# Performance work log

Hardware: AMD Instinct MI355X
Metric: run time of the kernel (lower is better)

## Reference

```python
import jax, jax.numpy as jnp
import numpy as np

BLOCK_SIZE = 256


def setup_inputs() -> dict:
    key = jax.random.key(0)
    k1, k2, k3, k4 = jax.random.split(key, 4)
    B, T, C, H = 512, 256, 384, 64
    x = jax.random.normal(k1, (B, T, C), dtype=jnp.float32)
    Wk = jax.random.normal(k2, (H, C), dtype=jnp.float32) * (1.0 / np.sqrt(C))
    Wq = jax.random.normal(k3, (H, C), dtype=jnp.float32) * (1.0 / np.sqrt(C))
    Wv = jax.random.normal(k4, (H, C), dtype=jnp.float32) * (1.0 / np.sqrt(C))
    return {"x": x, "Wk": Wk, "Wq": Wq, "Wv": Wv}


def reference(x, Wk, Wq, Wv):
    # x: [B, T, C]; Wk/Wq/Wv: [H, C] (torch nn.Linear weight layout, bias=False)
    B, T, C = x.shape
    H = Wk.shape[0]
    k = jnp.einsum('btc,hc->bth', x, Wk)
    q = jnp.einsum('btc,hc->bth', x, Wq)
    v = jnp.einsum('btc,hc->bth', x, Wv)
    scale = 1.0 / jnp.sqrt(jnp.float32(H))
    scores = jnp.einsum('bqh,bkh->bqk', q, k) * scale  # [B, T, T]
    causal = jnp.tril(jnp.ones((T, T), dtype=bool))
    scores = jnp.where(causal, scores, -jnp.inf)
    weights = jax.nn.softmax(scores, axis=-1)
    # dropout is identity in eval mode
    out = jnp.einsum('bqk,bkh->bqh', weights, v)  # [B, T, H]
    return out
```

## Files before the change

### kernel.cpp

```cpp
#include <hip/hip_runtime.h>
#include <hip/hip_bf16.h>
#include <math.h>

#define TT 256
#define CC 384
#define HH 64

typedef float v4f   __attribute__((ext_vector_type(4)));
typedef short short8 __attribute__((ext_vector_type(8)));

#define MFMA(a, b, c) __builtin_amdgcn_mfma_f32_16x16x32_bf16((a), (b), (c), 0, 0, 0)

__device__ __forceinline__ unsigned short f2bf(float f) {
    unsigned int u = __float_as_uint(f);
    u += 0x7FFFu + ((u >> 16) & 1u);
    return (unsigned short)(u >> 16);
}

__device__ __forceinline__ ushort4 f2bf4(float4 f) {
    union { __hip_bfloat162 h2[2]; ushort4 u4; } cv;
    cv.h2[0] = __float22bfloat162_rn(make_float2(f.x, f.y));
    cv.h2[1] = __float22bfloat162_rn(make_float2(f.z, f.w));
    return cv.u4;
}

__global__ __launch_bounds__(512, 4)
void qkv_proj(const float* __restrict__ x, const float* __restrict__ Wkp,
              const float* __restrict__ Wqp, const float* __restrict__ Wvp,
              unsigned short* __restrict__ qg, unsigned short* __restrict__ kg,
              unsigned short* __restrict__ vtg)
{
    __shared__ unsigned short sm[26112];
    unsigned short* x_s    = sm;
    unsigned short* w_s    = sm + 5120;
    unsigned short* epi_qk = sm;
    unsigned short* epi_vt = sm + 17408;

    const int tid  = threadIdx.x;
    const int wave = tid >> 6;
    const int lane = tid & 63;
    const int col  = lane & 15;
    const int quad = lane >> 4;
    const int row0 = blockIdx.x * 128;

    const int lr  = tid >> 3;
    const int lc4 = (tid & 7) * 4;

    const float* xp  = x   + (size_t)(row0 + lr) * CC + lc4;
    const float* wqp = Wqp + (size_t)lr * CC + lc4;
    const float* wkp = Wkp + (size_t)lr * CC + lc4;
    const float* wvp = Wvp + (size_t)lr * CC + lc4;

    v4f acc[12];
    #pragma unroll
    for (int j = 0; j < 12; ++j) acc[j] = (v4f){0.f, 0.f, 0.f, 0.f};

    float4 xA0 = *(const float4*)(xp);
    float4 xA1 = *(const float4*)(xp + 64 * CC);
    float4 wqA = *(const float4*)(wqp);
    float4 wkA = *(const float4*)(wkp);
    float4 wvA = *(const float4*)(wvp);

    const int afrag_off = (wave * 16 + col) * 40 + quad * 8;

    #pragma unroll
    for (int s = 0; s < 12; ++s) {
        float4 xB0, xB1, wqB, wkB, wvB;
        if (s < 11) {
            const int k0 = (s + 1) * 32;
            xB0 = *(const float4*)(xp + k0);
            xB1 = *(const float4*)(xp + 64 * CC + k0);
            wqB = *(const float4*)(wqp + k0);
            wkB = *(const float4*)(wkp + k0);
            wvB = *(const float4*)(wvp + k0);
        }
        __syncthreads();
        *(ushort4*)&x_s[lr * 40 + lc4]         = f2bf4(xA0);
        *(ushort4*)&x_s[(lr + 64) * 40 + lc4]  = f2bf4(xA1);
        *(ushort4*)&w_s[lr * 40 + lc4]         = f2bf4(wqA);
        *(ushort4*)&w_s[(64 + lr) * 40 + lc4]  = f2bf4(wkA);
        *(ushort4*)&w_s[(128 + lr) * 40 + lc4] = f2bf4(wvA);
        __syncthreads();
        const short8 a = *(const short8*)&x_s[afrag_off];
        #pragma unroll
        for (int nt = 0; nt < 12; ++nt) {
            const short8 bf = *(const short8*)&w_s[(nt * 16 + col) * 40 + quad * 8];
            acc[nt] = MFMA(a, bf, acc[nt]);
        }
        if (s < 11) { xA0 = xB0; xA1 = xB1; wqA = wqB; wkA = wkB; wvA = wvB; }
    }

    __syncthreads();
    #pragma unroll
    for (int nt = 0; nt < 12; ++nt) {
        #pragma unroll
        for (int r = 0; r < 4; ++r) {
            const int rl = wave * 16 + quad * 4 + r;
            const int n  = nt * 16 + col;
            const unsigned short hv = f2bf(acc[nt][r]);
            if (nt < 8) epi_qk[rl * 136 + n] = hv;
            else        epi_vt[(n - 128) * 136 + rl] = hv;
        }
    }
    __syncthreads();

    const int b    = row0 >> 8;
    const int half = (row0 >> 7) & 1;

    #pragma unroll
    for (int p = 0; p < 4; ++p) {
        const int idx = tid + p * 512;
        const int r = idx >> 4, ch = idx & 15;
        const short8 v = *(const short8*)&epi_qk[r * 136 + ch * 8];
        const size_t base = (size_t)(row0 + r) * 64 + (ch & 7) * 8;
        if (ch < 8) *(short8*)&qg[base] = v;
        else        *(short8*)&kg[base] = v;
    }
    #pragma unroll
    for (int p = 0; p < 2; ++p) {
        const int idx = tid + p * 512;
        const int h = idx >> 4, ch = idx & 15;
        const short8 v = *(const short8*)&epi_vt[h * 136 + ch * 8];
        *(short8*)&vtg[((size_t)b * 64 + h) * 256 + half * 128 + ch * 8] = v;
    }
}

__global__ __launch_bounds__(256, 4)
void attn(const unsigned short* __restrict__ qg, const unsigned short* __restrict__ kg,
          const unsigned short* __restrict__ vtg, float* __restrict__ out)
{
    __shared__ unsigned short Pb_all[4 * 16 * 40];
    const int tid  = threadIdx.x;
    const int wave = tid >> 6;
    const int lane = tid & 63;
    const int col  = lane & 15;
    const int quad = lane >> 4;
    const int b    = blockIdx.x >> 2;
    const int qt   = (blockIdx.x & 3) * 4 + wave;

    unsigned short* Pb = Pb_all + wave * 640;
    const unsigned short* kb_base = kg  + (size_t)b * 256 * 64;
    const unsigned short* vt_base = vtg + (size_t)b * 64 * 256;
    const float scale = 0.125f;

    const size_t qoff = ((size_t)b * 256 + qt * 16 + col) * 64 + quad * 8;
    const short8 aq0 = *(const short8*)(qg + qoff);
    const short8 aq1 = *(const short8*)(qg + qoff + 32);

    float lsum[4];
    v4f oacc[4];
    #pragma unroll
    for (int r = 0; r < 4; ++r) lsum[r] = 0.f;
    #pragma unroll
    for (int hn = 0; hn < 4; ++hn) oacc[hn] = (v4f){0.f, 0.f, 0.f, 0.f};

    const int nch = qt / 2 + 1;
    for (int kc = 0; kc < nch; ++kc) {
        const int kb = kc * 32;
        v4f s0 = (v4f){0.f, 0.f, 0.f, 0.f};
        v4f s1 = (v4f){0.f, 0.f, 0.f, 0.f};
        {
            const int ko0 = (kb + col) * 64 + quad * 8;
            const int ko1 = (kb + 16 + col) * 64 + quad * 8;
            const short8 b00 = *(const short8*)(kb_base + ko0);
            const short8 b01 = *(const short8*)(kb_base + ko0 + 32);
            const short8 b10 = *(const short8*)(kb_base + ko1);
            const short8 b11 = *(const short8*)(kb_base + ko1 + 32);
            s0 = MFMA(aq0, b00, s0);
            s0 = MFMA(aq1, b01, s0);
            s1 = MFMA(aq0, b10, s1);
            s1 = MFMA(aq1, b11, s1);
        }
        const bool diag = (kc == qt / 2);
        #pragma unroll
        for (int r = 0; r < 4; ++r) {
            const int t = qt * 16 + quad * 4 + r;
            float v0 = s0[r] * scale;
            float v1 = s1[r] * scale;
            if (diag) {
                if (kb + col > t)      v0 = -1e30f;
                if (kb + 16 + col > t) v1 = -1e30f;
            }
            const float p0 = __expf(v0);
            const float p1 = __expf(v1);
            lsum[r] += p0 + p1;
            Pb[(quad * 4 + r) * 40 + col]      = f2bf(p0);
            Pb[(quad * 4 + r) * 40 + 16 + col] = f2bf(p1);
        }
        __threadfence_block();
        const short8 ap = *(const short8*)&Pb[col * 40 + quad * 8];
        #pragma unroll
        for (int hn = 0; hn < 4; ++hn) {
            const short8 bv = *(const short8*)(vt_base + (hn * 16 + col) * 256 + kb + quad * 8);
            oacc[hn] = MFMA(ap, bv, oacc[hn]);
        }
    }

    #pragma unroll
    for (int r = 0; r < 4; ++r) {
        float l = lsum[r];
        l += __shfl_xor(l, 1);
        l += __shfl_xor(l, 2);
        l += __shfl_xor(l, 4);
        l += __shfl_xor(l, 8);
        const int t = qt * 16 + quad * 4 + r;
        const float inv = 1.0f / l;
        float* op = out + ((size_t)b * TT + t) * HH;
        #pragma unroll
        for (int hn = 0; hn < 4; ++hn)
            op[hn * 16 + col] = oacc[hn][r] * inv;
    }
}

extern "C" void kernel_launch(void* const* d_in, const int* in_sizes, int n_in,
                              void* d_out, int out_size, void* d_ws, size_t ws_size,
                              hipStream_t stream) {
    const float* x  = (const float*)d_in[0];
    const float* Wk = (const float*)d_in[1];
    const float* Wq = (const float*)d_in[2];
    const float* Wv = (const float*)d_in[3];
    float* out = (float*)d_out;

    unsigned short* qg  = (unsigned short*)d_ws;
    unsigned short* kg  = qg + (size_t)512 * 256 * 64;
    unsigned short* vtg = kg + (size_t)512 * 256 * 64;

    qkv_proj<<<dim3(1024), dim3(512), 0, stream>>>(x, Wk, Wq, Wv, qg, kg, vtg);
    attn<<<dim3(2048), dim3(256), 0, stream>>>(qg, kg, vtg, out);
}
```

Measured before the change: 359.8 us.

## Pair causal query tiles per wave, fold scale into Q, prefetch K

Each attention wave now processes two query tiles (j and 15-j), so causal work per wave is even, and the grid is halved. The softmax scale times log2(e) is folded into Q during the projection epilogue, which lets the attention kernel use exp2f with no per-element multiply. K fragments are prefetched one chunk ahead, and the projection epilogue reuses a smaller shared buffer in two phases to cut LDS use. Trade-offs: fewer blocks in flight, an extra barrier in the epilogue, and Q is rounded to bf16 after scaling.

```diff
diff --git a/kernel.cpp b/kernel.cpp
--- a/kernel.cpp
+++ b/kernel.cpp
@@ -23,6 +23,8 @@
     cv.h2[1] = __float22bfloat162_rn(make_float2(f.z, f.w));
     return cv.u4;
 }
+
+#define QSCALE 0.18033688f
 
 __global__ __launch_bounds__(512, 4)
 void qkv_proj(const float* __restrict__ x, const float* __restrict__ Wkp,
@@ -30,11 +32,10 @@
               unsigned short* __restrict__ qg, unsigned short* __restrict__ kg,
               unsigned short* __restrict__ vtg)
 {
-    __shared__ unsigned short sm[26112];
-    unsigned short* x_s    = sm;
-    unsigned short* w_s    = sm + 5120;
-    unsigned short* epi_qk = sm;
-    unsigned short* epi_vt = sm + 17408;
+    __shared__ unsigned short sm[17408];
+    unsigned short* x_s = sm;
+    unsigned short* w_s = sm + 5120;
+    unsigned short* epi = sm;
 
     const int tid  = threadIdx.x;
     const int wave = tid >> 6;
@@ -90,37 +91,48 @@
         if (s < 11) { xA0 = xB0; xA1 = xB1; wqA = wqB; wkA = wkB; wvA = wvB; }
     }
 
-    __syncthreads();
-    #pragma unroll
-    for (int nt = 0; nt < 12; ++nt) {
+    const int b    = row0 >> 8;
+    const int half = (row0 >> 7) & 1;
+
+    __syncthreads();
+    #pragma unroll
+    for (int nt = 0; nt < 8; ++nt) {
         #pragma unroll
         for (int r = 0; r < 4; ++r) {
             const int rl = wave * 16 + quad * 4 + r;
             const int n  = nt * 16 + col;
-            const unsigned short hv = f2bf(acc[nt][r]);
-            if (nt < 8) epi_qk[rl * 136 + n] = hv;
-            else        epi_vt[(n - 128) * 136 + rl] = hv;
-        }
-    }
-    __syncthreads();
-
-    const int b    = row0 >> 8;
-    const int half = (row0 >> 7) & 1;
-
+            float v = acc[nt][r];
+            if (nt < 4) v *= QSCALE;
+            epi[rl * 136 + n] = f2bf(v);
+        }
+    }
+    __syncthreads();
     #pragma unroll
     for (int p = 0; p < 4; ++p) {
         const int idx = tid + p * 512;
         const int r = idx >> 4, ch = idx & 15;
-        const short8 v = *(const short8*)&epi_qk[r * 136 + ch * 8];
+        const short8 v = *(const short8*)&epi[r * 136 + ch * 8];
         const size_t base = (size_t)(row0 + r) * 64 + (ch & 7) * 8;
         if (ch < 8) *(short8*)&qg[base] = v;
         else        *(short8*)&kg[base] = v;
     }
+
+    __syncthreads();
+    #pragma unroll
+    for (int nt = 8; nt < 12; ++nt) {
+        #pragma unroll
+        for (int r = 0; r < 4; ++r) {
+            const int rl = wave * 16 + quad * 4 + r;
+            const int h  = nt * 16 + col - 128;
+            epi[h * 136 + rl] = f2bf(acc[nt][r]);
+        }
+    }
+    __syncthreads();
     #pragma unroll
     for (int p = 0; p < 2; ++p) {
         const int idx = tid + p * 512;
         const int h = idx >> 4, ch = idx & 15;
-        const short8 v = *(const short8*)&epi_vt[h * 136 + ch * 8];
+        const short8 v = *(const short8*)&epi[h * 136 + ch * 8];
         *(short8*)&vtg[((size_t)b * 64 + h) * 256 + half * 128 + ch * 8] = v;
     }
 }
@@ -135,80 +147,93 @@
     const int lane = tid & 63;
     const int col  = lane & 15;
     const int quad = lane >> 4;
-    const int b    = blockIdx.x >> 2;
-    const int qt   = (blockIdx.x & 3) * 4 + wave;
+    const int b    = blockIdx.x >> 1;
+    const int g    = blockIdx.x & 1;
 
     unsigned short* Pb = Pb_all + wave * 640;
     const unsigned short* kb_base = kg  + (size_t)b * 256 * 64;
     const unsigned short* vt_base = vtg + (size_t)b * 64 * 256;
-    const float scale = 0.125f;
-
-    const size_t qoff = ((size_t)b * 256 + qt * 16 + col) * 64 + quad * 8;
-    const short8 aq0 = *(const short8*)(qg + qoff);
-    const short8 aq1 = *(const short8*)(qg + qoff + 32);
-
-    float lsum[4];
-    v4f oacc[4];
-    #pragma unroll
-    for (int r = 0; r < 4; ++r) lsum[r] = 0.f;
-    #pragma unroll
-    for (int hn = 0; hn < 4; ++hn) oacc[hn] = (v4f){0.f, 0.f, 0.f, 0.f};
-
-    const int nch = qt / 2 + 1;
-    for (int kc = 0; kc < nch; ++kc) {
-        const int kb = kc * 32;
-        v4f s0 = (v4f){0.f, 0.f, 0.f, 0.f};
-        v4f s1 = (v4f){0.f, 0.f, 0.f, 0.f};
+
+    #pragma unroll
+    for (int mi = 0; mi < 2; ++mi) {
+        const int j  = g * 4 + wave;
+        const int qt = mi ? (15 - j) : j;
+        const size_t qoff = ((size_t)b * 256 + qt * 16 + col) * 64 + quad * 8;
+        const short8 aq0 = *(const short8*)(qg + qoff);
+        const short8 aq1 = *(const short8*)(qg + qoff + 32);
+
+        float lsum[4];
+        v4f oacc[4];
+        #pragma unroll
+        for (int r = 0; r < 4; ++r) lsum[r] = 0.f;
+        #pragma unroll
+        for (int hn = 0; hn < 4; ++hn) oacc[hn] = (v4f){0.f, 0.f, 0.f, 0.f};
+
+        const int nch = qt / 2 + 1;
+        short8 b00, b01, b10, b11;
         {
-            const int ko0 = (kb + col) * 64 + quad * 8;
-            const int ko1 = (kb + 16 + col) * 64 + quad * 8;
-            const short8 b00 = *(const short8*)(kb_base + ko0);
-            const short8 b01 = *(const short8*)(kb_base + ko0 + 32);
-            const short8 b10 = *(const short8*)(kb_base + ko1);
-            const short8 b11 = *(const short8*)(kb_base + ko1 + 32);
+            const int ko0 = col * 64 + quad * 8;
+            const int ko1 = (16 + col) * 64 + quad * 8;
+            b00 = *(const short8*)(kb_base + ko0);
+            b01 = *(const short8*)(kb_base + ko0 + 32);
+            b10 = *(const short8*)(kb_base + ko1);
+            b11 = *(const short8*)(kb_base + ko1 + 32);
+        }
+        for (int kc = 0; kc < nch; ++kc) {
+            const int kb = kc * 32;
+            v4f s0 = (v4f){0.f, 0.f, 0.f, 0.f};
+            v4f s1 = (v4f){0.f, 0.f, 0.f, 0.f};
             s0 = MFMA(aq0, b00, s0);
             s0 = MFMA(aq1, b01, s0);
             s1 = MFMA(aq0, b10, s1);
             s1 = MFMA(aq1, b11, s1);
-        }
-        const bool diag = (kc == qt / 2);
+            if (kc + 1 < nch) {
+                const int ko0 = (kb + 32 + col) * 64 + quad * 8;
+                const int ko1 = (kb + 48 + col) * 64 + quad * 8;
+                b00 = *(const short8*)(kb_base + ko0);
+                b01 = *(const short8*)(kb_base + ko0 + 32);
+                b10 = *(const short8*)(kb_base + ko1);
+                b11 = *(const short8*)(kb_base + ko1 + 32);
+            }
+            const bool diag = (kc == qt / 2);
+            #pragma unroll
+            for (int r = 0; r < 4; ++r) {
+                const int t = qt * 16 + quad * 4 + r;
+                float v0 = s0[r];
+                float v1 = s1[r];
+                if (diag) {
+                    if (kb + col > t)      v0 = -1e30f;
+                    if (kb + 16 + col > t) v1 = -1e30f;
+                }
+                const float p0 = exp2f(v0);
+                const float p1 = exp2f(v1);
+                lsum[r] += p0 + p1;
+                Pb[(quad * 4 + r) * 40 + col]      = f2bf(p0);
+                Pb[(quad * 4 + r) * 40 + 16 + col] = f2bf(p1);
+            }
+            __threadfence_block();
+            const short8 ap = *(const short8*)&Pb[col * 40 + quad * 8];
+            #pragma unroll
+            for (int hn = 0; hn < 4; ++hn) {
+                const short8 bv = *(const short8*)(vt_base + (hn * 16 + col) * 256 + kb + quad * 8);
+                oacc[hn] = MFMA(ap, bv, oacc[hn]);
+            }
+        }
+
         #pragma unroll
         for (int r = 0; r < 4; ++r) {
+            float l = lsum[r];
+            l += __shfl_xor(l, 1);
+            l += __shfl_xor(l, 2);
+            l += __shfl_xor(l, 4);
+            l += __shfl_xor(l, 8);
             const int t = qt * 16 + quad * 4 + r;
-            float v0 = s0[r] * scale;
-            float v1 = s1[r] * scale;
-            if (diag) {
-                if (kb + col > t)      v0 = -1e30f;
-                if (kb + 16 + col > t) v1 = -1e30f;
-            }
-            const float p0 = __expf(v0);
-            const float p1 = __expf(v1);
-            lsum[r] += p0 + p1;
-            Pb[(quad * 4 + r) * 40 + col]      = f2bf(p0);
-            Pb[(quad * 4 + r) * 40 + 16 + col] = f2bf(p1);
-        }
-        __threadfence_block();
-        const short8 ap = *(const short8*)&Pb[col * 40 + quad * 8];
-        #pragma unroll
-        for (int hn = 0; hn < 4; ++hn) {
-            const short8 bv = *(const short8*)(vt_base + (hn * 16 + col) * 256 + kb + quad * 8);
-            oacc[hn] = MFMA(ap, bv, oacc[hn]);
-        }
-    }
-
-    #pragma unroll
-    for (int r = 0; r < 4; ++r) {
-        float l = lsum[r];
-        l += __shfl_xor(l, 1);
-        l += __shfl_xor(l, 2);
-        l += __shfl_xor(l, 4);
-        l += __shfl_xor(l, 8);
-        const int t = qt * 16 + quad * 4 + r;
-        const float inv = 1.0f / l;
-        float* op = out + ((size_t)b * TT + t) * HH;
-        #pragma unroll
-        for (int hn = 0; hn < 4; ++hn)
-            op[hn * 16 + col] = oacc[hn][r] * inv;
+            const float inv = 1.0f / l;
+            float* op = out + ((size_t)b * TT + t) * HH;
+            #pragma unroll
+            for (int hn = 0; hn < 4; ++hn)
+                op[hn * 16 + col] = oacc[hn][r] * inv;
+        }
     }
 }
 
@@ -226,5 +251,5 @@
     unsigned short* vtg = kg + (size_t)512 * 256 * 64;
 
     qkv_proj<<<dim3(1024), dim3(512), 0, stream>>>(x, Wk, Wq, Wv, qg, kg, vtg);
-    attn<<<dim3(2048), dim3(256), 0, stream>>>(qg, kg, vtg, out);
-}
+    attn<<<dim3(1024), dim3(256), 0, stream>>>(qg, kg, vtg, out);
+}
```

After: 335.4 us. 1.07x faster.
